# Performance work log

Hardware: AMD Instinct MI355X
Metric: run time of the kernel (lower is better)

## Reference

```python
import jax, jax.numpy as jnp
import numpy as np

TF = 512  # text_features
VF = 512  # video_features


def setup_inputs() -> dict:
    key = jax.random.key(0)
    k1, k2, k3 = jax.random.split(key, 3)
    text = jax.random.normal(k1, (4, 32, TF), dtype=jnp.float32)
    video = jax.random.normal(k2, (4, 64, 196, VF), dtype=jnp.float32)
    # nn.Linear(text_features + video_features, 1): weight (1, TF+VF), bias (1,)
    w = jax.random.normal(k3, (TF + VF,), dtype=jnp.float32) * (1.0 / np.sqrt(TF + VF))
    b = jnp.zeros((1,), dtype=jnp.float32)
    return {"text": text, "video": video, "w": w, "b": b}


def reference(text, video, w, b):
    # Split the 1-output linear over the concat into text-only and video-only
    # projections: Linear(cat([t, v])) = t @ wt + v @ wv + b  (exact algebra).
    tf = text.shape[-1]
    wt, wv = w[:tf], w[tf:]
    score_t = jnp.einsum('btf,f->bt', text, wt) + b[0]        # (B, St)
    score_v = jnp.einsum('bvhf,f->bvh', video, wv)            # (B, Sv, HW)
    scores = score_t[:, :, None, None] + score_v[:, None]     # (B, St, Sv, HW)
    B, St, Sv, HW = scores.shape
    # softmax over the flattened (Sv*HW) dim, per (b, st)
    weights = jax.nn.softmax(scores.reshape(B, St, Sv * HW), axis=-1)
    weights = weights.reshape(B, St, Sv, HW)
    # fused[b,st,sv,f] = sum_hw weights[b,st,sv,hw] * video[b,sv,hw,f]
    fused = jnp.einsum('bsvh,bvhf->bsvf', weights, video)
    return fused
```

## Files before the change

kernel.cpp:

```cpp
#include <hip/hip_runtime.h>

#define TF 512
#define VF 512
#define BB 4
#define ST 32
#define SV 64
#define HW 196
#define ROWS_PER_B (SV * HW)
#define NROW (BB * ROWS_PER_B)

__global__ __launch_bounds__(256) void score_kernel(const float4* __restrict__ video,
                                                    const float* __restrict__ w,
                                                    float* __restrict__ scores) {
    int gwave = (blockIdx.x * blockDim.x + threadIdx.x) >> 6;
    int lane  = threadIdx.x & 63;
    if (gwave >= NROW) return;
    const float4* row = video + (size_t)gwave * (VF / 4);
    const float4* wv4 = (const float4*)(w + TF);
    float4 a0 = row[lane];
    float4 a1 = row[lane + 64];
    float4 w0 = wv4[lane];
    float4 w1 = wv4[lane + 64];
    float s = a0.x * w0.x + a0.y * w0.y + a0.z * w0.z + a0.w * w0.w
            + a1.x * w1.x + a1.y * w1.y + a1.z * w1.z + a1.w * w1.w;
    #pragma unroll
    for (int off = 32; off > 0; off >>= 1)
        s += __shfl_down(s, off, 64);
    if (lane == 0) scores[gwave] = s;
}

__global__ __launch_bounds__(1024) void softmax_kernel(float* __restrict__ scores) {
    int b = blockIdx.x;
    float* s = scores + (size_t)b * ROWS_PER_B;
    int tid = threadIdx.x;
    __shared__ float red[16];
    __shared__ float bstat;

    float m = -INFINITY;
    for (int i = tid; i < ROWS_PER_B; i += 1024) m = fmaxf(m, s[i]);
    #pragma unroll
    for (int off = 32; off > 0; off >>= 1) m = fmaxf(m, __shfl_down(m, off, 64));
    if ((tid & 63) == 0) red[tid >> 6] = m;
    __syncthreads();
    if (tid == 0) {
        float mm = red[0];
        #pragma unroll
        for (int i = 1; i < 16; i++) mm = fmaxf(mm, red[i]);
        bstat = mm;
    }
    __syncthreads();
    m = bstat;
    __syncthreads();

    float sum = 0.0f;
    for (int i = tid; i < ROWS_PER_B; i += 1024) {
        float e = expf(s[i] - m);
        s[i] = e;
        sum += e;
    }
    #pragma unroll
    for (int off = 32; off > 0; off >>= 1) sum += __shfl_down(sum, off, 64);
    if ((tid & 63) == 0) red[tid >> 6] = sum;
    __syncthreads();
    if (tid == 0) {
        float ss = 0.0f;
        #pragma unroll
        for (int i = 0; i < 16; i++) ss += red[i];
        bstat = 1.0f / ss;
    }
    __syncthreads();
    float inv = bstat;

    for (int i = tid; i < ROWS_PER_B; i += 1024) s[i] *= inv;
}

__global__ __launch_bounds__(256) void fuse_kernel(const float4* __restrict__ video,
                                                   const float* __restrict__ weights,
                                                   float4* __restrict__ out) {
    int bv = blockIdx.x;
    int b = bv >> 6;
    int v = bv & 63;
    int tid = threadIdx.x;
    __shared__ float wsh[HW];
    __shared__ float4 accsh[VF / 4];

    if (tid < HW) wsh[tid] = weights[bv * HW + tid];
    __syncthreads();

    const float4* vrow = video + (size_t)bv * HW * (VF / 4);
    int f    = tid & 127;
    int half = tid >> 7;
    float4 acc = make_float4(0.f, 0.f, 0.f, 0.f);
    for (int h = half; h < HW; h += 2) {
        float wh = wsh[h];
        float4 x = vrow[h * (VF / 4) + f];
        acc.x = fmaf(wh, x.x, acc.x);
        acc.y = fmaf(wh, x.y, acc.y);
        acc.z = fmaf(wh, x.z, acc.z);
        acc.w = fmaf(wh, x.w, acc.w);
    }
    if (half) accsh[f] = acc;
    __syncthreads();
    if (!half) {
        float4 o = accsh[f];
        acc.x += o.x; acc.y += o.y; acc.z += o.z; acc.w += o.w;
        accsh[f] = acc;
    }
    __syncthreads();
    float4 res = accsh[f];

    int s0 = half * 16;
    #pragma unroll
    for (int s = 0; s < 16; s++) {
        size_t idx = (((size_t)(b * ST + s0 + s)) * SV + v) * (VF / 4) + f;
        out[idx] = res;
    }
}

extern "C" void kernel_launch(void* const* d_in, const int* in_sizes, int n_in,
                              void* d_out, int out_size, void* d_ws, size_t ws_size,
                              hipStream_t stream) {
    const float* video = (const float*)d_in[1];
    const float* w     = (const float*)d_in[2];
    float* scores = (float*)d_ws;

    score_kernel<<<NROW / 4, 256, 0, stream>>>((const float4*)video, w, scores);
    softmax_kernel<<<BB, 1024, 0, stream>>>(scores);
    fuse_kernel<<<BB * SV, 256, 0, stream>>>((const float4*)video, scores,
                                             (float4*)d_out);
}
```

Measured before the change: 193.4 us.

## Fold softmax into score and fuse kernels using unshifted exp and partial sums

Removes the separate 4-block softmax kernel. The score kernel now writes exp(score) and per-block partial sums. The fuse kernel reduces those partials itself and scales its weighted sum by the reciprocal, and it uses 512 threads split over four hw quarters. This removes a poorly parallel launch and its passes over the scores. It drops the max subtraction, so exp can overflow for large scores.

```diff
diff --git a/kernel.cpp b/kernel.cpp
--- a/kernel.cpp
+++ b/kernel.cpp
@@ -8,13 +8,15 @@
 #define HW 196
 #define ROWS_PER_B (SV * HW)
 #define NROW (BB * ROWS_PER_B)
+#define PART_PER_B (ROWS_PER_B / 4)
 
 __global__ __launch_bounds__(256) void score_kernel(const float4* __restrict__ video,
                                                     const float* __restrict__ w,
-                                                    float* __restrict__ scores) {
-    int gwave = (blockIdx.x * blockDim.x + threadIdx.x) >> 6;
-    int lane  = threadIdx.x & 63;
-    if (gwave >= NROW) return;
+                                                    float* __restrict__ escore,
+                                                    float* __restrict__ partial) {
+    int tid   = threadIdx.x;
+    int gwave = (blockIdx.x * 256 + tid) >> 6;
+    int lane  = tid & 63;
     const float4* row = video + (size_t)gwave * (VF / 4);
     const float4* wv4 = (const float4*)(w + TF);
     float4 a0 = row[lane];
@@ -26,72 +28,50 @@
     #pragma unroll
     for (int off = 32; off > 0; off >>= 1)
         s += __shfl_down(s, off, 64);
-    if (lane == 0) scores[gwave] = s;
+
+    __shared__ float ps[4];
+    if (lane == 0) {
+        float e = __expf(s);
+        escore[gwave] = e;
+        ps[tid >> 6] = e;
+    }
+    __syncthreads();
+    if (tid == 0)
+        partial[blockIdx.x] = ps[0] + ps[1] + ps[2] + ps[3];
 }
 
-__global__ __launch_bounds__(1024) void softmax_kernel(float* __restrict__ scores) {
-    int b = blockIdx.x;
-    float* s = scores + (size_t)b * ROWS_PER_B;
+__global__ __launch_bounds__(512) void fuse_kernel(const float4* __restrict__ video,
+                                                   const float* __restrict__ escore,
+                                                   const float* __restrict__ partial,
+                                                   float4* __restrict__ out) {
+    int bv  = blockIdx.x;
+    int b   = bv >> 6;
+    int v   = bv & 63;
     int tid = threadIdx.x;
-    __shared__ float red[16];
-    __shared__ float bstat;
 
-    float m = -INFINITY;
-    for (int i = tid; i < ROWS_PER_B; i += 1024) m = fmaxf(m, s[i]);
+    __shared__ float red[8];
+    __shared__ float wsh[HW];
+    __shared__ float4 accsh[4][128];
+
+    const float* pb = partial + b * PART_PER_B;
+    float local = 0.0f;
+    for (int i = tid; i < PART_PER_B; i += 512) local += pb[i];
     #pragma unroll
-    for (int off = 32; off > 0; off >>= 1) m = fmaxf(m, __shfl_down(m, off, 64));
-    if ((tid & 63) == 0) red[tid >> 6] = m;
-    __syncthreads();
-    if (tid == 0) {
-        float mm = red[0];
-        #pragma unroll
-        for (int i = 1; i < 16; i++) mm = fmaxf(mm, red[i]);
-        bstat = mm;
-    }
-    __syncthreads();
-    m = bstat;
+    for (int off = 32; off > 0; off >>= 1) local += __shfl_down(local, off, 64);
+    if ((tid & 63) == 0) red[tid >> 6] = local;
+
+    if (tid < HW) wsh[tid] = escore[bv * HW + tid];
     __syncthreads();
 
-    float sum = 0.0f;
-    for (int i = tid; i < ROWS_PER_B; i += 1024) {
-        float e = expf(s[i] - m);
-        s[i] = e;
-        sum += e;
-    }
-    #pragma unroll
-    for (int off = 32; off > 0; off >>= 1) sum += __shfl_down(sum, off, 64);
-    if ((tid & 63) == 0) red[tid >> 6] = sum;
-    __syncthreads();
-    if (tid == 0) {
-        float ss = 0.0f;
-        #pragma unroll
-        for (int i = 0; i < 16; i++) ss += red[i];
-        bstat = 1.0f / ss;
-    }
-    __syncthreads();
-    float inv = bstat;
-
-    for (int i = tid; i < ROWS_PER_B; i += 1024) s[i] *= inv;
-}
-
-__global__ __launch_bounds__(256) void fuse_kernel(const float4* __restrict__ video,
-                                                   const float* __restrict__ weights,
-                                                   float4* __restrict__ out) {
-    int bv = blockIdx.x;
-    int b = bv >> 6;
-    int v = bv & 63;
-    int tid = threadIdx.x;
-    __shared__ float wsh[HW];
-    __shared__ float4 accsh[VF / 4];
-
-    if (tid < HW) wsh[tid] = weights[bv * HW + tid];
-    __syncthreads();
+    float tot = red[0] + red[1] + red[2] + red[3]
+              + red[4] + red[5] + red[6] + red[7];
+    float inv = 1.0f / tot;
 
     const float4* vrow = video + (size_t)bv * HW * (VF / 4);
-    int f    = tid & 127;
-    int half = tid >> 7;
+    int f = tid & 127;
+    int q = tid >> 7;
     float4 acc = make_float4(0.f, 0.f, 0.f, 0.f);
-    for (int h = half; h < HW; h += 2) {
+    for (int h = q; h < HW; h += 4) {
         float wh = wsh[h];
         float4 x = vrow[h * (VF / 4) + f];
         acc.x = fmaf(wh, x.x, acc.x);
@@ -99,20 +79,19 @@
         acc.z = fmaf(wh, x.z, acc.z);
         acc.w = fmaf(wh, x.w, acc.w);
     }
-    if (half) accsh[f] = acc;
+    accsh[q][f] = acc;
     __syncthreads();
-    if (!half) {
-        float4 o = accsh[f];
-        acc.x += o.x; acc.y += o.y; acc.z += o.z; acc.w += o.w;
-        accsh[f] = acc;
-    }
-    __syncthreads();
-    float4 res = accsh[f];
 
-    int s0 = half * 16;
+    float4 r0 = accsh[0][f], r1 = accsh[1][f], r2 = accsh[2][f], r3 = accsh[3][f];
+    float4 res;
+    res.x = (r0.x + r1.x + r2.x + r3.x) * inv;
+    res.y = (r0.y + r1.y + r2.y + r3.y) * inv;
+    res.z = (r0.z + r1.z + r2.z + r3.z) * inv;
+    res.w = (r0.w + r1.w + r2.w + r3.w) * inv;
+
     #pragma unroll
-    for (int s = 0; s < 16; s++) {
-        size_t idx = (((size_t)(b * ST + s0 + s)) * SV + v) * (VF / 4) + f;
+    for (int s = 0; s < 8; s++) {
+        size_t idx = (((size_t)(b * ST + q * 8 + s)) * SV + v) * (VF / 4) + f;
         out[idx] = res;
     }
 }
@@ -122,10 +101,11 @@
                               hipStream_t stream) {
     const float* video = (const float*)d_in[1];
     const float* w     = (const float*)d_in[2];
-    float* scores = (float*)d_ws;
+    float* escore  = (float*)d_ws;
+    float* partial = escore + NROW;
 
-    score_kernel<<<NROW / 4, 256, 0, stream>>>((const float4*)video, w, scores);
-    softmax_kernel<<<BB, 1024, 0, stream>>>(scores);
-    fuse_kernel<<<BB * SV, 256, 0, stream>>>((const float4*)video, scores,
-                                             (float4*)d_out);
+    score_kernel<<<NROW / 4, 256, 0, stream>>>((const float4*)video, w,
+                                               escore, partial);
+    fuse_kernel<<<BB * SV, 512, 0, stream>>>((const float4*)video, escore,
+                                             partial, (float4*)d_out);
 }
```

Result: faster. 174.3 us (-9.9%).
